# Optimization experiments

Measured on AMD Instinct MI355X. Metric: run time of the kernel, lower is better.

Reference implementation:

```python
import jax, jax.numpy as jnp
import numpy as np
import math

B, I, O, C = 8192, 1024, 1024, 6


def setup_inputs() -> dict:
    key = jax.random.key(0)
    k1, k2, k3, k4 = jax.random.split(key, 4)
    inputs = jax.random.normal(k1, (B, I), dtype=jnp.float32)
    phase_radians = jax.random.uniform(k2, (B,), dtype=jnp.float32) * (2.0 * math.pi)
    # xavier-uniform per control point: bound = sqrt(6/(I+O))
    bound = math.sqrt(6.0 / (I + O))
    weight_control_points = jax.random.uniform(k3, (C, O, I), dtype=jnp.float32, minval=-bound, maxval=bound)
    bias_control_points = jnp.zeros((C, O), dtype=jnp.float32) + 0.01 * jax.random.normal(k4, (C, O), dtype=jnp.float32)
    return {"inputs": inputs, "phase_radians": phase_radians,
            "weight_control_points": weight_control_points,
            "bias_control_points": bias_control_points}


def _catmull_rom(phase_radians, num_control_points):
    two_pi = 2.0 * math.pi
    phase = jnp.remainder(phase_radians, two_pi)
    position = phase * (float(num_control_points) / two_pi)
    base = jnp.floor(position)
    base_idx = base.astype(jnp.int32)
    t = position - base
    t2 = t * t
    t3 = t2 * t
    indices = jnp.stack([
        jnp.remainder(base_idx - 1, num_control_points),
        jnp.remainder(base_idx, num_control_points),
        jnp.remainder(base_idx + 1, num_control_points),
        jnp.remainder(base_idx + 2, num_control_points),
    ], axis=1)  # [B, 4]
    weights = jnp.stack([
        -0.5 * t + t2 - 0.5 * t3,
        1.0 - 2.5 * t2 + 1.5 * t3,
        0.5 * t + 2.0 * t2 - 1.5 * t3,
        -0.5 * t2 + 0.5 * t3,
    ], axis=1)  # [B, 4]
    return indices, weights


def reference(inputs, phase_radians, weight_control_points, bias_control_points):
    # Faithful to: out[b] = sum_k w[b,k] * (W[idx[b,k]] @ x[b] + bias[idx[b,k]])
    # Instead of materializing [B,O,I] interpolated weights, compute all C
    # control-point projections once and gather the 4 needed per sample.
    num_cp = weight_control_points.shape[0]
    indices, cr_weights = _catmull_rom(phase_radians.astype(inputs.dtype), num_cp)
    y_all = jnp.einsum('coi,bi->bco', weight_control_points, inputs)  # [B, C, O]
    y_sel = jnp.take_along_axis(y_all, indices[:, :, None], axis=1)  # [B, 4, O]
    b_sel = bias_control_points[indices]                              # [B, 4, O]
    return jnp.einsum('bk,bko->bo', cr_weights, y_sel + b_sel)
```

## Files before the change

### kernel.cpp

```cpp
#include <hip/hip_runtime.h>
#include <hip/hip_bf16.h>
#include <math.h>

#define B_SZ 8192
#define I_SZ 1024
#define O_SZ 1024
#define NCP  6

typedef __attribute__((ext_vector_type(8))) short bf16x8;
typedef __attribute__((ext_vector_type(4))) float f32x4;

__device__ __forceinline__ unsigned short f2bf(float f) {
  union { float f; unsigned int u; } v; v.f = f;
  unsigned int u = v.u;
  u += 0x7FFFu + ((u >> 16) & 1u);
  return (unsigned short)(u >> 16);
}

__device__ __forceinline__ int seg_of(float ph) {
  const float two_pi = 6.2831855f;
  const float scale = (float)(6.0 / 6.283185307179586);
  float pm = fmodf(ph, two_pi);
  int bi = (int)floorf(pm * scale);
  return ((bi % NCP) + NCP) % NCP;
}

__global__ __launch_bounds__(1024) void prep_w_sort(
    const float* __restrict__ w, unsigned short* __restrict__ wb, int n4,
    const float* __restrict__ phase,
    unsigned short* __restrict__ perm,
    int* __restrict__ blkinfo) {
  __shared__ int scanbuf[1024][NCP];
  __shared__ int ownh[1024][NCP];
  __shared__ int cum[NCP + 1];
  int t = (int)threadIdx.x;

  if ((int)blockIdx.x != (int)gridDim.x - 1) {
    int idx = blockIdx.x * 1024 + t;
    int stride = ((int)gridDim.x - 1) * 1024;
    for (int i = idx; i < n4; i += stride) {
      float4 v = reinterpret_cast<const float4*>(w)[i];
      ushort4 o;
      o.x = f2bf(v.x); o.y = f2bf(v.y); o.z = f2bf(v.z); o.w = f2bf(v.w);
      reinterpret_cast<ushort4*>(wb)[i] = o;
    }
    return;
  }

  int segs[8];
#pragma unroll
  for (int s = 0; s < NCP; ++s) scanbuf[t][s] = 0;
#pragma unroll
  for (int i = 0; i < 8; ++i) {
    segs[i] = seg_of(phase[t * 8 + i]);
    scanbuf[t][segs[i]]++;
  }
#pragma unroll
  for (int s = 0; s < NCP; ++s) ownh[t][s] = scanbuf[t][s];
  __syncthreads();
  for (int d = 1; d < 1024; d <<= 1) {
    int add[NCP];
    if (t >= d) {
#pragma unroll
      for (int s = 0; s < NCP; ++s) add[s] = scanbuf[t - d][s];
    }
    __syncthreads();
    if (t >= d) {
#pragma unroll
      for (int s = 0; s < NCP; ++s) scanbuf[t][s] += add[s];
    }
    __syncthreads();
  }
  if (t == 0) {
    cum[0] = 0;
    for (int s = 0; s < NCP; ++s) cum[s + 1] = cum[s] + scanbuf[1023][s];
  }
  __syncthreads();
#pragma unroll
  for (int s = 0; s < NCP; ++s)
    ownh[t][s] = cum[s] + scanbuf[t][s] - ownh[t][s];
#pragma unroll
  for (int i = 0; i < 8; ++i) {
    int s = segs[i];
    perm[ownh[t][s]++] = (unsigned short)(t * 8 + i);
  }
  if (t < B_SZ / 256) {
    int start = t * 256, end = start + 255;
    int s0 = 0; while (s0 < NCP - 1 && cum[s0 + 1] <= start) ++s0;
    int s1 = 0; while (s1 < NCP - 1 && cum[s1 + 1] <= end) ++s1;
    int nj = s1 - s0 + 4; if (nj > NCP) nj = NCP;
    blkinfo[2 * t] = (s0 + NCP - 1) % NCP;
    blkinfo[2 * t + 1] = nj;
  }
}

__global__ void cast_x_perm(const float* __restrict__ x,
                            const unsigned short* __restrict__ perm,
                            unsigned short* __restrict__ xb) {
  int idx = blockIdx.x * blockDim.x + threadIdx.x;
  int stride = gridDim.x * blockDim.x;
  const int total = B_SZ * (I_SZ / 4);
  for (int i = idx; i < total; i += stride) {
    int pos = i >> 8;
    int c = i & 255;
    int src = (int)perm[pos];
    float4 v = reinterpret_cast<const float4*>(x + (size_t)src * I_SZ)[c];
    ushort4 o;
    o.x = f2bf(v.x); o.y = f2bf(v.y); o.z = f2bf(v.z); o.w = f2bf(v.w);
    reinterpret_cast<ushort4*>(xb + (size_t)pos * I_SZ)[c] = o;
  }
}

__device__ __forceinline__ void gload_lds16(const void* g, void* l) {
  __builtin_amdgcn_global_load_lds(
      (const __attribute__((address_space(1))) void*)g,
      (__attribute__((address_space(3))) void*)l, 16, 0, 0);
}

#define BM 256
#define BN 128
#define BK 64
#define NBUF 3

__global__ __launch_bounds__(512, 1) void pfl_gemm(
    const unsigned short* __restrict__ xb,
    const unsigned short* __restrict__ wb,
    const float* __restrict__ phase,
    const unsigned short* __restrict__ perm,
    const int* __restrict__ blkinfo,
    const float* __restrict__ bias,
    float* __restrict__ out) {
  __shared__ __align__(16) unsigned short Abuf[NBUF][BM * BK];
  __shared__ __align__(16) unsigned short Bbuf[NBUF][BN * BK];
  __shared__ __align__(16) float c4[NCP][BM];
  __shared__ int pblk[BM];

  const int nbn = O_SZ / BN;
  int bid = (int)blockIdx.x;
  int swz = (bid & 7) * 32 + (bid >> 3);
  int rowblk = swz / nbn;
  int brow = rowblk * BM;
  int bcol = (swz % nbn) * BN;

  int tid = (int)threadIdx.x;
  int lane = tid & 63;
  int wid = tid >> 6;
  int wr = wid >> 1;
  int wc = wid & 1;

  int jlo = blkinfo[2 * rowblk];
  int NTb = blkinfo[2 * rowblk + 1] << 4;

  if (tid < BM) {
    int orow = (int)perm[brow + tid];
    pblk[tid] = orow;
    float ph = phase[orow];
    const float two_pi = 6.2831855f;
    float pm = fmodf(ph, two_pi);
    float pos = pm * (float)(6.0 / 6.283185307179586);
    float base = floorf(pos);
    int bi = (int)base;
    float t = pos - base;
    float t2 = t * t, t3 = t2 * t;
    float w0 = -0.5f * t + t2 - 0.5f * t3;
    float w1 = 1.0f - 2.5f * t2 + 1.5f * t3;
    float w2 = 0.5f * t + 2.0f * t2 - 1.5f * t3;
    float w3 = -0.5f * t2 + 0.5f * t3;
    float cc[NCP] = {0.f, 0.f, 0.f, 0.f, 0.f, 0.f};
    cc[((bi - 1) % NCP + NCP) % NCP] += w0;
    cc[(bi % NCP + NCP) % NCP]       += w1;
    cc[((bi + 1) % NCP + NCP) % NCP] += w2;
    cc[((bi + 2) % NCP + NCP) % NCP] += w3;
    for (int j = 0; j < NCP; ++j) c4[j][tid] = cc[j];
  }

  f32x4 acc[4][4];
  f32x4 part[4][4];
#pragma unroll
  for (int m = 0; m < 4; ++m)
#pragma unroll
    for (int n = 0; n < 4; ++n) {
      acc[m][n] = (f32x4){0.f, 0.f, 0.f, 0.f};
      part[m][n] = (f32x4){0.f, 0.f, 0.f, 0.f};
    }

  int swzcol = ((lane & 7) ^ (lane >> 3)) * 8;
  const unsigned short* xsrc =
      xb + (size_t)(brow + wid * 8 + (lane >> 3)) * I_SZ + swzcol;
  const unsigned short* wsrc =
      wb + (size_t)(bcol + wid * 8 + (lane >> 3)) * I_SZ + swzcol;

  int lbase = (lane & 15) * 128 + (((lane >> 4) ^ (lane & 7)) & 7) * 16;

  auto STAGE = [&](int t, int b) {
    int ks = (t & 15) * 64;
    int cN = jlo + (t >> 4); if (cN >= NCP) cN -= NCP;
    const unsigned short* xs = xsrc + ks;
    const unsigned short* ws = wsrc + (size_t)cN * O_SZ * I_SZ + ks;
    unsigned short* Ad = &Abuf[b][(wid * 8) * BK];
    unsigned short* Bd = &Bbuf[b][(wid * 8) * BK];
#pragma unroll
    for (int p = 0; p < 4; ++p)
      gload_lds16(xs + (size_t)p * 64 * I_SZ, Ad + p * 64 * BK);
#pragma unroll
    for (int p = 0; p < 2; ++p)
      gload_lds16(ws + (size_t)p * 64 * I_SZ, Bd + p * 64 * BK);
  };

  STAGE(0, 0);
  STAGE(1, 1);
  asm volatile("s_waitcnt vmcnt(6)" ::: "memory");
  __builtin_amdgcn_sched_barrier(0);
  __syncthreads();

  int cur = 0;
  for (int t = 0; t < NTb; ++t) {
    const char* Ab = (const char*)&Abuf[cur][0];
    const char* Bb = (const char*)&Bbuf[cur][0];
    int st = cur + 2; if (st >= NBUF) st -= NBUF;

    bf16x8 af0[4], bf0[4], af1[4], bf1[4];
#pragma unroll
    for (int m = 0; m < 4; ++m)
      af0[m] = *reinterpret_cast<const bf16x8*>(
          Ab + (wr * 64 + m * 16) * 128 + lbase);
#pragma unroll
    for (int n = 0; n < 4; ++n)
      bf0[n] = *reinterpret_cast<const bf16x8*>(
          Bb + (wc * 64 + n * 16) * 128 + lbase);
    if (t + 2 < NTb) STAGE(t + 2, st);
    asm volatile("s_waitcnt lgkmcnt(0)" ::: "memory");
    __builtin_amdgcn_sched_barrier(0);

#pragma unroll
    for (int m = 0; m < 4; ++m)
      af1[m] = *reinterpret_cast<const bf16x8*>(
          Ab + (wr * 64 + m * 16) * 128 + (lbase ^ 64));
#pragma unroll
    for (int n = 0; n < 4; ++n)
      bf1[n] = *reinterpret_cast<const bf16x8*>(
          Bb + (wc * 64 + n * 16) * 128 + (lbase ^ 64));
    __builtin_amdgcn_sched_barrier(0);

    __builtin_amdgcn_s_setprio(1);
#pragma unroll
    for (int m = 0; m < 4; ++m)
#pragma unroll
      for (int n = 0; n < 4; ++n)
        part[m][n] = __builtin_amdgcn_mfma_f32_16x16x32_bf16(
            af0[m], bf0[n], part[m][n], 0, 0, 0);
    __builtin_amdgcn_s_setprio(0);

    asm volatile("s_waitcnt lgkmcnt(0)" ::: "memory");
    __builtin_amdgcn_sched_barrier(0);

    __builtin_amdgcn_s_setprio(1);
#pragma unroll
    for (int m = 0; m < 4; ++m)
#pragma unroll
      for (int n = 0; n < 4; ++n)
        part[m][n] = __builtin_amdgcn_mfma_f32_16x16x32_bf16(
            af1[m], bf1[n], part[m][n], 0, 0, 0);
    __builtin_amdgcn_s_setprio(0);

    if ((t & 15) == 15) {
      int cj = jlo + (t >> 4); if (cj >= NCP) cj -= NCP;
#pragma unroll
      for (int m = 0; m < 4; ++m) {
        f32x4 cv = *reinterpret_cast<const f32x4*>(
            &c4[cj][wr * 64 + m * 16 + (lane >> 4) * 4]);
#pragma unroll
        for (int n = 0; n < 4; ++n) {
          acc[m][n] += cv * part[m][n];
          part[m][n] = (f32x4){0.f, 0.f, 0.f, 0.f};
        }
      }
    }

    if (t + 2 < NTb)
      asm volatile("s_waitcnt vmcnt(6)" ::: "memory");
    else
      asm volatile("s_waitcnt vmcnt(0)" ::: "memory");
    __builtin_amdgcn_sched_barrier(0);
    __builtin_amdgcn_s_barrier();
    ++cur; if (cur == NBUF) cur = 0;
  }

#pragma unroll
  for (int n = 0; n < 4; ++n) {
    int col = bcol + wc * 64 + n * 16 + (lane & 15);
    float b6[NCP];
#pragma unroll
    for (int j = 0; j < NCP; ++j) b6[j] = bias[j * O_SZ + col];
#pragma unroll
    for (int m = 0; m < 4; ++m) {
#pragma unroll
      for (int r = 0; r < 4; ++r) {
        int rloc = wr * 64 + m * 16 + (lane >> 4) * 4 + r;
        float s = 0.f;
#pragma unroll
        for (int j = 0; j < NCP; ++j) s += c4[j][rloc] * b6[j];
        out[(size_t)pblk[rloc] * O_SZ + col] = acc[m][n][r] + s;
      }
    }
  }
}

extern "C" void kernel_launch(void* const* d_in, const int* in_sizes, int n_in,
                              void* d_out, int out_size, void* d_ws, size_t ws_size,
                              hipStream_t stream) {
  (void)in_sizes; (void)n_in; (void)out_size; (void)ws_size;
  const float* x     = (const float*)d_in[0];
  const float* phase = (const float*)d_in[1];
  const float* w     = (const float*)d_in[2];
  const float* bias  = (const float*)d_in[3];
  float* out = (float*)d_out;

  char* ws = (char*)d_ws;
  unsigned short* xb = (unsigned short*)ws;
  unsigned short* wb = (unsigned short*)(ws + (size_t)16 * 1024 * 1024);
  unsigned short* perm = (unsigned short*)(ws + (size_t)28 * 1024 * 1024);
  int* blkinfo = (int*)(ws + (size_t)28 * 1024 * 1024 + 16384);

  prep_w_sort<<<769, 1024, 0, stream>>>(w, wb, NCP * O_SZ * I_SZ / 4,
                                        phase, perm, blkinfo);
  cast_x_perm<<<2048, 256, 0, stream>>>(x, perm, xb);

  dim3 grid((B_SZ / BM) * (O_SZ / BN));
  pfl_gemm<<<grid, 512, 0, stream>>>(xb, wb, phase, perm, blkinfo, bias, out);
}
```

Before: 113.1 us.

## Merge x cast into prep kernel and gather permuted rows inside GEMM

The separate permuted cast of x is removed. x is now cast to bf16 in original order inside one merged prep kernel alongside the weight cast and the phase sort. The GEMM instead looks up perm to compute per-row source pointers and gathers the permuted rows during its global-to-LDS loads. This drops one kernel launch and removes the dependency of the x cast on the sort. The cost is that A-tile loads become row-gathered instead of contiguous, which may reduce locality.

```diff
diff --git a/kernel.cpp b/kernel.cpp
--- a/kernel.cpp
+++ b/kernel.cpp
@@ -25,8 +25,9 @@
   return ((bi % NCP) + NCP) % NCP;
 }
 
-__global__ __launch_bounds__(1024) void prep_w_sort(
-    const float* __restrict__ w, unsigned short* __restrict__ wb, int n4,
+__global__ __launch_bounds__(1024) void prep_all(
+    const float* __restrict__ x, unsigned short* __restrict__ xb,
+    const float* __restrict__ w, unsigned short* __restrict__ wb,
     const float* __restrict__ phase,
     unsigned short* __restrict__ perm,
     int* __restrict__ blkinfo) {
@@ -34,11 +35,23 @@
   __shared__ int ownh[1024][NCP];
   __shared__ int cum[NCP + 1];
   int t = (int)threadIdx.x;
-
-  if ((int)blockIdx.x != (int)gridDim.x - 1) {
-    int idx = blockIdx.x * 1024 + t;
-    int stride = ((int)gridDim.x - 1) * 1024;
-    for (int i = idx; i < n4; i += stride) {
+  int b = (int)blockIdx.x;
+
+  if (b < 1024) {
+    const int n4 = B_SZ * I_SZ / 4;
+    int idx = b * 1024 + t;
+    for (int i = idx; i < n4; i += 1024 * 1024) {
+      float4 v = reinterpret_cast<const float4*>(x)[i];
+      ushort4 o;
+      o.x = f2bf(v.x); o.y = f2bf(v.y); o.z = f2bf(v.z); o.w = f2bf(v.w);
+      reinterpret_cast<ushort4*>(xb)[i] = o;
+    }
+    return;
+  }
+  if (b < 2048) {
+    const int n4 = NCP * O_SZ * I_SZ / 4;
+    int idx = (b - 1024) * 1024 + t;
+    for (int i = idx; i < n4; i += 1024 * 1024) {
       float4 v = reinterpret_cast<const float4*>(w)[i];
       ushort4 o;
       o.x = f2bf(v.x); o.y = f2bf(v.y); o.z = f2bf(v.z); o.w = f2bf(v.w);
@@ -91,23 +104,6 @@
     int nj = s1 - s0 + 4; if (nj > NCP) nj = NCP;
     blkinfo[2 * t] = (s0 + NCP - 1) % NCP;
     blkinfo[2 * t + 1] = nj;
-  }
-}
-
-__global__ void cast_x_perm(const float* __restrict__ x,
-                            const unsigned short* __restrict__ perm,
-                            unsigned short* __restrict__ xb) {
-  int idx = blockIdx.x * blockDim.x + threadIdx.x;
-  int stride = gridDim.x * blockDim.x;
-  const int total = B_SZ * (I_SZ / 4);
-  for (int i = idx; i < total; i += stride) {
-    int pos = i >> 8;
-    int c = i & 255;
-    int src = (int)perm[pos];
-    float4 v = reinterpret_cast<const float4*>(x + (size_t)src * I_SZ)[c];
-    ushort4 o;
-    o.x = f2bf(v.x); o.y = f2bf(v.y); o.z = f2bf(v.z); o.w = f2bf(v.w);
-    reinterpret_cast<ushort4*>(xb + (size_t)pos * I_SZ)[c] = o;
   }
 }
 
@@ -185,8 +181,11 @@
     }
 
   int swzcol = ((lane & 7) ^ (lane >> 3)) * 8;
-  const unsigned short* xsrc =
-      xb + (size_t)(brow + wid * 8 + (lane >> 3)) * I_SZ + swzcol;
+  int r0 = brow + wid * 8 + (lane >> 3);
+  const unsigned short* xsP0 = xb + (size_t)perm[r0      ] * I_SZ + swzcol;
+  const unsigned short* xsP1 = xb + (size_t)perm[r0 +  64] * I_SZ + swzcol;
+  const unsigned short* xsP2 = xb + (size_t)perm[r0 + 128] * I_SZ + swzcol;
+  const unsigned short* xsP3 = xb + (size_t)perm[r0 + 192] * I_SZ + swzcol;
   const unsigned short* wsrc =
       wb + (size_t)(bcol + wid * 8 + (lane >> 3)) * I_SZ + swzcol;
 
@@ -195,16 +194,15 @@
   auto STAGE = [&](int t, int b) {
     int ks = (t & 15) * 64;
     int cN = jlo + (t >> 4); if (cN >= NCP) cN -= NCP;
-    const unsigned short* xs = xsrc + ks;
     const unsigned short* ws = wsrc + (size_t)cN * O_SZ * I_SZ + ks;
     unsigned short* Ad = &Abuf[b][(wid * 8) * BK];
     unsigned short* Bd = &Bbuf[b][(wid * 8) * BK];
-#pragma unroll
-    for (int p = 0; p < 4; ++p)
-      gload_lds16(xs + (size_t)p * 64 * I_SZ, Ad + p * 64 * BK);
-#pragma unroll
-    for (int p = 0; p < 2; ++p)
-      gload_lds16(ws + (size_t)p * 64 * I_SZ, Bd + p * 64 * BK);
+    gload_lds16(xsP0 + ks, Ad);
+    gload_lds16(xsP1 + ks, Ad + 64 * BK);
+    gload_lds16(xsP2 + ks, Ad + 128 * BK);
+    gload_lds16(xsP3 + ks, Ad + 192 * BK);
+    gload_lds16(ws, Bd);
+    gload_lds16(ws + (size_t)64 * I_SZ, Bd + 64 * BK);
   };
 
   STAGE(0, 0);
@@ -322,9 +320,7 @@
   unsigned short* perm = (unsigned short*)(ws + (size_t)28 * 1024 * 1024);
   int* blkinfo = (int*)(ws + (size_t)28 * 1024 * 1024 + 16384);
 
-  prep_w_sort<<<769, 1024, 0, stream>>>(w, wb, NCP * O_SZ * I_SZ / 4,
-                                        phase, perm, blkinfo);
-  cast_x_perm<<<2048, 256, 0, stream>>>(x, perm, xb);
+  prep_all<<<2049, 1024, 0, stream>>>(x, xb, w, wb, phase, perm, blkinfo);
 
   dim3 grid((B_SZ / BM) * (O_SZ / BN));
   pfl_gemm<<<grid, 512, 0, stream>>>(xb, wb, phase, perm, blkinfo, bias, out);
```

After: 110.8 us. 1.02x faster.
